# Kernel optimization log

Measured on AMD Instinct MI355X. Metric: run time of the kernel, lower is better.

## Reference

```python
import jax, jax.numpy as jnp
import numpy as np

H, DH = 12, 64
EPS = 1e-6
ROPE_BASE = 100.0

def rms_norm(x, scale=None, eps=EPS):
    xf = x.astype(jnp.float32)
    n = xf * jax.lax.rsqrt(jnp.mean(xf * xf, axis=-1, keepdims=True) + eps)
    if scale is not None:
        n = n * scale.astype(jnp.float32)
    return n.astype(x.dtype)

def rotate_half(x):
    h = x.shape[-1] // 2
    return jnp.concatenate([-x[..., h:], x[..., :h]], axis=-1)

def rope_cos_sin(pos_ids, head_dim, base=ROPE_BASE):
    # pos_ids: [B, N, 2] int -> cos/sin [B, N, head_dim]
    dim = head_dim // 2
    inv = 1.0 / base ** (jnp.arange(0, dim, 2, dtype=jnp.float32) / dim)  # [dim//2]
    cos_l, sin_l = [], []
    for i in range(2):  # x and y coordinate
        pos = pos_ids[:, :, i].astype(jnp.float32)           # [B, N]
        freqs = pos[:, :, None] * inv[None, None, :]          # [B, N, dim//2]
        emb = jnp.concatenate([freqs, freqs], axis=-1)        # [B, N, dim]
        cos_l.append(jnp.cos(emb))
        sin_l.append(jnp.sin(emb))
    return jnp.concatenate(cos_l, axis=-1), jnp.concatenate(sin_l, axis=-1)

def apply_2d_rope(x, cos, sin):
    # x: [B, N, H, Dh]; cos/sin: [B, N, Dh]; split channels evenly between x/y.
    c = x.shape[-1] // 2
    outs = []
    for k in range(2):
        xs = x[..., k * c:(k + 1) * c]
        cc = cos[:, :, None, k * c:(k + 1) * c]
        ss = sin[:, :, None, k * c:(k + 1) * c]
        outs.append(xs * cc + rotate_half(xs) * ss)
    return jnp.concatenate(outs, axis=-1)

def setup_inputs() -> dict:
    key = jax.random.key(0)
    ks = jax.random.split(key, 7)
    B, N, D = 8, 1024, 768
    hidden_states = jax.random.normal(ks[0], (B, N, D), dtype=jnp.float32)
    pixel_position_ids = jax.random.randint(ks[1], (B, N, 2), 0, 32, dtype=jnp.int32)
    s = 0.02
    Wq = jax.random.normal(ks[2], (H * DH, D), dtype=jnp.float32) * s
    Wk = jax.random.normal(ks[3], (H * DH, D), dtype=jnp.float32) * s
    Wv = jax.random.normal(ks[4], (H * DH, D), dtype=jnp.float32) * s
    Wo = jax.random.normal(ks[5], (D, H * DH), dtype=jnp.float32) * s
    q_scale = jnp.ones((DH,), dtype=jnp.float32)
    k_scale = jnp.ones((DH,), dtype=jnp.float32)
    return {"hidden_states": hidden_states, "pixel_position_ids": pixel_position_ids,
            "Wq": Wq, "Wk": Wk, "Wv": Wv, "Wo": Wo,
            "q_scale": q_scale, "k_scale": k_scale}

def reference(hidden_states, pixel_position_ids, Wq, Wk, Wv, Wo, q_scale, k_scale):
    B, N, D = hidden_states.shape
    # QKV projections (clip bounds are +/-inf -> no-op). Weights are [out, in].
    q = (hidden_states @ Wq.T).reshape(B, N, H, DH)
    k = (hidden_states @ Wk.T).reshape(B, N, H, DH)
    v = (hidden_states @ Wv.T).reshape(B, N, H, DH)
    # Per-head RMSNorm (v has no learned scale)
    q = rms_norm(q, q_scale)
    k = rms_norm(k, k_scale)
    v = rms_norm(v, None)
    # 2D RoPE
    cos, sin = rope_cos_sin(pixel_position_ids, DH)
    q = apply_2d_rope(q, cos, sin)
    k = apply_2d_rope(k, cos, sin)
    # Full attention, scaling = 1.0, softmax in fp32
    scores = jnp.einsum('bqhd,bkhd->bhqk', q, k)
    attn = jax.nn.softmax(scores.astype(jnp.float32), axis=-1).astype(q.dtype)
    out = jnp.einsum('bhqk,bkhd->bqhd', attn, v).reshape(B, N, H * DH)
    return out @ Wo.T
```

## Files before the change

### kernel.cpp

```cpp
#include <hip/hip_runtime.h>

typedef _Float16 f16;
typedef __attribute__((ext_vector_type(8))) _Float16 f16x8;
typedef __attribute__((ext_vector_type(4))) _Float16 f16x4;
typedef __attribute__((ext_vector_type(2))) __fp16 h16x2;
typedef __attribute__((ext_vector_type(4))) float f32x4;

#define NH 12
#define DHD 64
#define NB 8
#define NSEQ 1024
#define DMODEL 768
#define BHN (NB*NH)
#define ROWS_PER (BHN*NSEQ)

#define MFMA(a,b,c) __builtin_amdgcn_mfma_f32_16x16x32_f16(a,b,c,0,0,0)

__device__ __forceinline__ void gload16(const void* g, void* l) {
  __builtin_amdgcn_global_load_lds(
      (__attribute__((address_space(1))) void*)(g),
      (__attribute__((address_space(3))) void*)(l), 16, 0, 0);
}

__global__ __launch_bounds__(256) void cast_all_kernel(const float* __restrict__ hs,
                                                       const float* __restrict__ Wq,
                                                       const float* __restrict__ Wk,
                                                       const float* __restrict__ Wv,
                                                       const float* __restrict__ Wo,
                                                       f16* __restrict__ Xf,
                                                       f16* __restrict__ Wf,
                                                       f16* __restrict__ Wof,
                                                       float2* __restrict__ rtab,
                                                       int nhs, int nw) {
  int i = (blockIdx.x * blockDim.x + threadIdx.x) * 4;
  const float* src;
  f16* dst;
  if (i < nhs) {
    src = hs + i; dst = Xf + i;
  } else {
    int j = i - nhs;
    int which = j / nw;
    int off = j - which*nw;
    src = ((which == 0) ? Wq : (which == 1) ? Wk : (which == 2) ? Wv : Wo) + off;
    dst = ((which < 3) ? (Wf + (size_t)which*nw) : Wof) + off;
  }
  float4 v = *(const float4*)src;
  f16x4 o = {(f16)v.x, (f16)v.y, (f16)v.z, (f16)v.w};
  *(f16x4*)dst = o;
  if (blockIdx.x == 0) {
    for (int e = threadIdx.x; e < 512; e += 256) {
      int pos = e >> 4, k = e & 15;
      float ang = (float)pos * __expf((float)k * (-4.605170185988091f / 16.0f));
      float sn, cs;
      __sincosf(ang, &sn, &cs);
      rtab[e] = make_float2(cs, sn);
    }
  }
}

template<int MODE>
__global__ __launch_bounds__(512) void gemm_bt(const f16* __restrict__ A,
                                               const f16* __restrict__ B,
                                               float* __restrict__ Cout,
                                               f16* __restrict__ QKout,
                                               f16* __restrict__ Vout,
                                               const int* __restrict__ pos_ids,
                                               const float* __restrict__ q_scale,
                                               const float* __restrict__ k_scale,
                                               const float2* __restrict__ rtab,
                                               int M, int N, int K) {
  constexpr int BN = (MODE == 1) ? 128 : 64;
  constexpr int NJ = BN / 32;
  constexpr int ABUF = 8192;
  constexpr int BBUF = BN*64;
  __shared__ __align__(16) f16 SH[2*ABUF + 2*BBUF];
  const int tid = threadIdx.x;
  const int w = tid >> 6, l = tid & 63;
  const int wr = w >> 1, wc = w & 1;
  const int g = l >> 4, i16 = l & 15;

  int bx, by;
  {
    int id = blockIdx.x;
    const int nbx = (MODE == 1) ? 18 : 12;
    const int chunk = (MODE == 1) ? 144 : 96;
    int idp = (id & 7) * chunk + (id >> 3);
    by = idp / nbx; bx = idp - by * nbx;
  }

  const f32x4 fzero = {0.f, 0.f, 0.f, 0.f};
  f32x4 acc[2][NJ];
#pragma unroll
  for (int i = 0; i < 2; i++)
#pragma unroll
    for (int j = 0; j < NJ; j++) acc[i][j] = fzero;

  const int srow = tid >> 3;
  const int schunk = (tid & 7) ^ (srow & 7);
  const size_t arow = (size_t)(by*128 + srow)*K + schunk*8;
  const size_t brow = (size_t)(bx*BN + srow)*K + schunk*8;

  const int nt = K / 64;
#define STAGE(buf, k0)                                                          \
  {                                                                             \
    char* AlB = (char*)(SH + (buf)*ABUF) + w*1024;                              \
    char* BlB = (char*)(SH + 2*ABUF + (buf)*BBUF) + w*1024;                     \
    _Pragma("unroll")                                                           \
    for (int n = 0; n < 2; ++n)                                                 \
      gload16(A + arow + (size_t)(n*64)*K + (k0), AlB + n*8192);                \
    _Pragma("unroll")                                                           \
    for (int n = 0; n < BN/64; ++n)                                             \
      gload16(B + brow + (size_t)(n*64)*K + (k0), BlB + n*8192);                \
  }

  STAGE(0, 0);
  __syncthreads();
  for (int t = 0; t < nt; ++t) {
    const int buf = t & 1;
    if (t + 1 < nt) STAGE(buf ^ 1, (t + 1)*64);
    const f16* Ac = SH + buf*ABUF;
    const f16* Bc = SH + 2*ABUF + buf*BBUF;
#pragma unroll
    for (int kk = 0; kk < 2; ++kk) {
      f16x8 af[2], bfr[NJ];
#pragma unroll
      for (int i = 0; i < 2; i++)
        af[i] = *(const f16x8*)(Ac + (wr*32 + i*16 + i16)*64 + ((kk*4 + g) ^ (i16 & 7))*8);
#pragma unroll
      for (int j = 0; j < NJ; j++)
        bfr[j] = *(const f16x8*)(Bc + (wc*(BN/2) + j*16 + i16)*64 + ((kk*4 + g) ^ (i16 & 7))*8);
#pragma unroll
      for (int i = 0; i < 2; i++)
#pragma unroll
        for (int j = 0; j < NJ; j++)
          acc[i][j] = MFMA(af[i], bfr[j], acc[i][j]);
    }
    __syncthreads();
  }
#undef STAGE

  const int m0 = by*128 + wr*32;
  const int n0 = bx*BN + wc*(BN/2);
  if constexpr (MODE == 0) {
#pragma unroll
    for (int i = 0; i < 2; i++)
#pragma unroll
      for (int j = 0; j < NJ; j++)
#pragma unroll
        for (int r = 0; r < 4; r++) {
          int m = m0 + i*16 + g*4 + r;
          int n = n0 + j*16 + i16;
          Cout[(size_t)m*N + n] = acc[i][j][r];
        }
  } else {
  if (bx >= 12) {
    const int h0 = (bx - 12)*2;
    const int bb = by >> 3;
    const int ns0 = (by & 7) * 128;
    f16* Lt = SH;
#pragma unroll
    for (int i = 0; i < 2; i++) {
      f32x4 ssv = fzero;
#pragma unroll
      for (int j = 0; j < 4; j++)
#pragma unroll
        for (int r = 0; r < 4; r++) ssv[r] += acc[i][j][r]*acc[i][j][r];
#pragma unroll
      for (int d = 1; d < 16; d <<= 1)
#pragma unroll
        for (int r = 0; r < 4; r++) ssv[r] += __shfl_xor(ssv[r], d);
#pragma unroll
      for (int r = 0; r < 4; r++) {
        float rinv = rsqrtf(ssv[r] * (1.0f/64.0f) + 1e-6f);
        int nsl = wr*32 + i*16 + g*4 + r;
#pragma unroll
        for (int j = 0; j < 4; j++)
          Lt[(wc*64 + j*16 + i16)*136 + nsl] = (f16)(acc[i][j][r]*rinv);
      }
    }
    __syncthreads();
    const int dh = tid >> 2, q4 = tid & 3;
    f16* dst = Vout + ((size_t)((bb*NH + h0 + (dh >> 6))*64 + (dh & 63)))*1024
               + ns0 + q4*32;
    const f16* ls = Lt + dh*136 + q4*32;
#pragma unroll
    for (int e = 0; e < 4; ++e)
      *(uint4*)(dst + e*8) = *(const uint4*)(ls + e*8);
  } else {
    const int qkv = n0 / DMODEL;
    const int h = (n0 - qkv*DMODEL) >> 6;
    const float* scp = (qkv == 0) ? q_scale : k_scale;
    float scl[4];
#pragma unroll
    for (int j = 0; j < 4; j++) {
      scl[j] = scp[j*16 + i16];
      if (qkv == 0) scl[j] *= 1.4426950408889634f;
    }
    const float2* rt = rtab + i16;
#pragma unroll
    for (int i = 0; i < 2; i++) {
      f32x4 ssv = fzero;
#pragma unroll
      for (int j = 0; j < 4; j++)
#pragma unroll
        for (int r = 0; r < 4; r++) ssv[r] += acc[i][j][r]*acc[i][j][r];
#pragma unroll
      for (int d = 1; d < 16; d <<= 1)
#pragma unroll
        for (int r = 0; r < 4; r++) ssv[r] += __shfl_xor(ssv[r], d);
#pragma unroll
      for (int r = 0; r < 4; r++) {
        int m = m0 + i*16 + g*4 + r;
        int bb = m >> 10, ns = m & 1023;
        float rinv = rsqrtf(ssv[r] * (1.0f/64.0f) + 1e-6f);
        int2 pp = *(const int2*)(pos_ids + ((size_t)bb*NSEQ + ns)*2);
        float2 t0 = rt[pp.x*16];
        float2 t1 = rt[pp.y*16];
        float x0 = acc[i][0][r]*rinv*scl[0];
        float x1 = acc[i][1][r]*rinv*scl[1];
        float x2 = acc[i][2][r]*rinv*scl[2];
        float x3 = acc[i][3][r]*rinv*scl[3];
        size_t row = ((size_t)qkv*BHN + bb*NH + h)*NSEQ + ns;
        f16* ob = QKout + row*64;
        ob[i16]      = (f16)(x0*t0.x - x1*t0.y);
        ob[16 + i16] = (f16)(x1*t0.x + x0*t0.y);
        ob[32 + i16] = (f16)(x2*t1.x - x3*t1.y);
        ob[48 + i16] = (f16)(x3*t1.x + x2*t1.y);
      }
    }
  }
  }
}

__device__ __forceinline__ int sigma_perm(int p) {
  return (p & 0x20) | ((p & 0xC) << 1) | ((p & 0x10) >> 2) | (p & 3);
}

#define FM3(a,b,c) fmaxf(fmaxf(a,b),c)

__global__ __launch_bounds__(512) void attn_kernel(const f16* __restrict__ QKu,
                                                   const f16* __restrict__ Vtu,
                                                   f16* __restrict__ O) {
  const int id = blockIdx.x;
  const int xcd = id & 7, idx = id >> 3;
  const int bh = xcd*12 + (idx >> 3);
  const int q0 = (idx & 7) * 128;
  const int tid = threadIdx.x, w = tid >> 6, l = tid & 63;
  const int g = l >> 4, i16 = l & 15;
  const int g4 = g*4;
  const int sw = i16 & 7;
  const int b = bh / NH, h = bh - b*NH;

  __shared__ __align__(16) f16 Ks[2*64*64];
  __shared__ __align__(16) f16 Vs[2*64*64];

  const f16* qrow = QKu + ((size_t)bh*NSEQ + q0 + w*16 + i16)*64;
  f16x8 q0f = *(const f16x8*)(qrow + g*8);
  f16x8 q1f = *(const f16x8*)(qrow + 32 + g*8);

  const char* Kb  = (const char*)(QKu + (size_t)(BHN + bh)*NSEQ*64);
  const char* Vtb = (const char*)(Vtu + (size_t)bh*64*1024);
  const int prow0 = w*8 + (l >> 3);
  const int cl = (l & 7) ^ (l >> 3);
  const char* Ksrc = Kb + sigma_perm(prow0)*128 + cl*16;
  const char* Vsrc = Vtb + prow0*2048 + cl*16;

  const f32x4 fzero = {0.f, 0.f, 0.f, 0.f};
  const f16x8 vones = {(f16)1.f,(f16)1.f,(f16)1.f,(f16)1.f,
                       (f16)1.f,(f16)1.f,(f16)1.f,(f16)1.f};
  float mR = -1e30f;
  f32x4 o[4];
  f32x4 acc_l = fzero;
#pragma unroll
  for (int t = 0; t < 4; t++) o[t] = fzero;

  int cur = 0;
  {
    gload16(Ksrc, (char*)Ks + w*1024);
    gload16(Vsrc, (char*)Vs + w*1024);
  }
  __syncthreads();

  for (int t = 0; t < 16; ++t) {
    if (t < 15) {
      gload16(Ksrc + (t+1)*8192, (char*)Ks + (cur^1)*8192 + w*1024);
      gload16(Vsrc + (t+1)*128,  (char*)Vs + (cur^1)*8192 + w*1024);
    }
    const f16* Kc = Ks + cur*4096;
    const f16* Vc = Vs + cur*4096;

    f32x4 s[4] = {fzero, fzero, fzero, fzero};
    __builtin_amdgcn_s_setprio(1);
#pragma unroll
    for (int j = 0; j < 4; ++j) {
      const f16* kr = Kc + (j*16 + i16)*64;
      f16x8 k0 = *(const f16x8*)(kr + (g ^ sw)*8);
      f16x8 k1 = *(const f16x8*)(kr + ((g^4) ^ sw)*8);
      s[j] = MFMA(k0, q0f, s[j]);
      s[j] = MFMA(k1, q1f, s[j]);
    }
    __builtin_amdgcn_s_setprio(0);

    float t0m = FM3(s[0][0], s[0][1], s[0][2]);
    float t1m = FM3(s[0][3], s[1][0], s[1][1]);
    float t2m = FM3(s[1][2], s[1][3], s[2][0]);
    float t3m = FM3(s[2][1], s[2][2], s[2][3]);
    float t4m = FM3(s[3][0], s[3][1], s[3][2]);
    float tm = fmaxf(FM3(FM3(t0m, t1m, t2m), t3m, t4m), s[3][3]);
    tm = fmaxf(tm, __shfl_xor(tm, 16));
    tm = fmaxf(tm, __shfl_xor(tm, 32));
    if (__any(tm > mR + 11.5416f)) {
      float nm = fmaxf(mR, tm);
      float fac = __builtin_amdgcn_exp2f(mR - nm);
      mR = nm;
#pragma unroll
      for (int r = 0; r < 4; ++r) {
        float fr = __shfl(fac, g4 + r);
        o[0][r] *= fr; o[1][r] *= fr; o[2][r] *= fr; o[3][r] *= fr;
        acc_l[r] *= fr;
      }
    }
#pragma unroll
    for (int j = 0; j < 4; ++j)
#pragma unroll
      for (int r = 0; r < 4; ++r) s[j][r] = __builtin_amdgcn_exp2f(s[j][r] - mR);

    union { h16x2 h[4]; f16x8 v; } u0, u1;
    u0.h[0] = __builtin_amdgcn_cvt_pkrtz(s[0][0], s[0][1]);
    u0.h[1] = __builtin_amdgcn_cvt_pkrtz(s[0][2], s[0][3]);
    u0.h[2] = __builtin_amdgcn_cvt_pkrtz(s[1][0], s[1][1]);
    u0.h[3] = __builtin_amdgcn_cvt_pkrtz(s[1][2], s[1][3]);
    u1.h[0] = __builtin_amdgcn_cvt_pkrtz(s[2][0], s[2][1]);
    u1.h[1] = __builtin_amdgcn_cvt_pkrtz(s[2][2], s[2][3]);
    u1.h[2] = __builtin_amdgcn_cvt_pkrtz(s[3][0], s[3][1]);
    u1.h[3] = __builtin_amdgcn_cvt_pkrtz(s[3][2], s[3][3]);
    f16x8 pa0 = u0.v, pa1 = u1.v;

    __builtin_amdgcn_s_setprio(1);
#pragma unroll
    for (int t2 = 0; t2 < 4; ++t2) {
      const f16* vr = Vc + (t2*16 + i16)*64;
      f16x8 bv0 = *(const f16x8*)(vr + (g ^ sw)*8);
      f16x8 bv1 = *(const f16x8*)(vr + ((g^4) ^ sw)*8);
      o[t2] = MFMA(pa0, bv0, o[t2]);
      o[t2] = MFMA(pa1, bv1, o[t2]);
    }
    acc_l = MFMA(pa0, vones, acc_l);
    acc_l = MFMA(pa1, vones, acc_l);
    __builtin_amdgcn_s_setprio(0);

    __syncthreads();
    cur ^= 1;
  }

#pragma unroll
  for (int r = 0; r < 4; ++r) {
    float invl = 1.0f / acc_l[r];
    int q = q0 + w*16 + g4 + r;
    size_t base = ((size_t)(b*NSEQ + q))*DMODEL + h*DHD;
#pragma unroll
    for (int t2 = 0; t2 < 4; ++t2)
      O[base + t2*16 + i16] = (f16)(o[t2][r] * invl);
  }
}

extern "C" void kernel_launch(void* const* d_in, const int* in_sizes, int n_in,
                              void* d_out, int out_size, void* d_ws, size_t ws_size,
                              hipStream_t stream) {
  const float* hs = (const float*)d_in[0];
  const int*   pos = (const int*)d_in[1];
  const float* Wq = (const float*)d_in[2];
  const float* Wk = (const float*)d_in[3];
  const float* Wv = (const float*)d_in[4];
  const float* Wo = (const float*)d_in[5];
  const float* qs = (const float*)d_in[6];
  const float* ks = (const float*)d_in[7];

  const int nhs = 8192*768;
  const int nw  = 768*768;

  char* p = (char*)d_ws;
  f16* Xf   = (f16*)p; p += (size_t)nhs*2;
  f16* Wf   = (f16*)p; p += (size_t)3*nw*2;
  f16* Wof  = (f16*)p; p += (size_t)nw*2;
  f16* QKpk = (f16*)p; p += (size_t)2*ROWS_PER*64*2;
  f16* Vt   = (f16*)p; p += (size_t)ROWS_PER*64*2;
  f16* Ob   = (f16*)p; p += (size_t)nhs*2;
  float2* Rtab = (float2*)p; p += 512*sizeof(float2);

  cast_all_kernel<<<(nhs + 4*nw)/1024, 256, 0, stream>>>(hs, Wq, Wk, Wv, Wo,
                                                         Xf, Wf, Wof, Rtab, nhs, nw);

  gemm_bt<1><<<1152, 512, 0, stream>>>(Xf, Wf, nullptr, QKpk, Vt,
                                       pos, qs, ks, Rtab, 8192, 2304, 768);
  attn_kernel<<<768, 512, 0, stream>>>(QKpk, Vt, Ob);
  gemm_bt<0><<<768, 512, 0, stream>>>(Ob, Wof, (float*)d_out, nullptr, nullptr,
                                      nullptr, nullptr, nullptr, nullptr, 8192, 768, 768);
}
```

Baseline: 111.3 us.

## Triple-buffer QKV GEMM LDS pipeline with explicit vmcnt waits

For the QKV projection GEMM (MODE 1), the shared-memory staging goes from double to triple buffering. Two tiles are prefetched ahead, and waits are done with explicit s_waitcnt vmcnt(4) plus raw barriers in place of __syncthreads. This lets global-to-LDS loads for tile t+2 overlap compute on tile t and avoids draining all outstanding loads every iteration. It raises LDS usage per block, which may lower occupancy, and it relies on hand-counted vmcnt values being correct.

```diff
diff --git a/kernel.cpp b/kernel.cpp
--- a/kernel.cpp
+++ b/kernel.cpp
@@ -73,7 +73,8 @@
   constexpr int NJ = BN / 32;
   constexpr int ABUF = 8192;
   constexpr int BBUF = BN*64;
-  __shared__ __align__(16) f16 SH[2*ABUF + 2*BBUF];
+  constexpr int NBUF = (MODE == 1) ? 3 : 2;
+  __shared__ __align__(16) f16 SH[NBUF*(ABUF + BBUF)];
   const int tid = threadIdx.x;
   const int w = tid >> 6, l = tid & 63;
   const int wr = w >> 1, wc = w & 1;
@@ -104,7 +105,7 @@
 #define STAGE(buf, k0)                                                          \
   {                                                                             \
     char* AlB = (char*)(SH + (buf)*ABUF) + w*1024;                              \
-    char* BlB = (char*)(SH + 2*ABUF + (buf)*BBUF) + w*1024;                     \
+    char* BlB = (char*)(SH + NBUF*ABUF + (buf)*BBUF) + w*1024;                  \
     _Pragma("unroll")                                                           \
     for (int n = 0; n < 2; ++n)                                                 \
       gload16(A + arow + (size_t)(n*64)*K + (k0), AlB + n*8192);                \
@@ -112,32 +113,62 @@
     for (int n = 0; n < BN/64; ++n)                                             \
       gload16(B + brow + (size_t)(n*64)*K + (k0), BlB + n*8192);                \
   }
-
-  STAGE(0, 0);
-  __syncthreads();
-  for (int t = 0; t < nt; ++t) {
-    const int buf = t & 1;
-    if (t + 1 < nt) STAGE(buf ^ 1, (t + 1)*64);
-    const f16* Ac = SH + buf*ABUF;
-    const f16* Bc = SH + 2*ABUF + buf*BBUF;
-#pragma unroll
-    for (int kk = 0; kk < 2; ++kk) {
-      f16x8 af[2], bfr[NJ];
-#pragma unroll
-      for (int i = 0; i < 2; i++)
-        af[i] = *(const f16x8*)(Ac + (wr*32 + i*16 + i16)*64 + ((kk*4 + g) ^ (i16 & 7))*8);
-#pragma unroll
-      for (int j = 0; j < NJ; j++)
-        bfr[j] = *(const f16x8*)(Bc + (wc*(BN/2) + j*16 + i16)*64 + ((kk*4 + g) ^ (i16 & 7))*8);
-#pragma unroll
-      for (int i = 0; i < 2; i++)
-#pragma unroll
-        for (int j = 0; j < NJ; j++)
-          acc[i][j] = MFMA(af[i], bfr[j], acc[i][j]);
-    }
+#define COMPUTE(buf)                                                            \
+  {                                                                             \
+    const f16* Ac = SH + (buf)*ABUF;                                            \
+    const f16* Bc = SH + NBUF*ABUF + (buf)*BBUF;                                \
+    _Pragma("unroll")                                                           \
+    for (int kk = 0; kk < 2; ++kk) {                                            \
+      f16x8 af[2], bfr[NJ];                                                     \
+      _Pragma("unroll")                                                         \
+      for (int i = 0; i < 2; i++)                                               \
+        af[i] = *(const f16x8*)(Ac + (wr*32 + i*16 + i16)*64 +                  \
+                                ((kk*4 + g) ^ (i16 & 7))*8);                    \
+      _Pragma("unroll")                                                         \
+      for (int j = 0; j < NJ; j++)                                              \
+        bfr[j] = *(const f16x8*)(Bc + (wc*(BN/2) + j*16 + i16)*64 +             \
+                                 ((kk*4 + g) ^ (i16 & 7))*8);                   \
+      _Pragma("unroll")                                                         \
+      for (int i = 0; i < 2; i++)                                               \
+        _Pragma("unroll")                                                       \
+        for (int j = 0; j < NJ; j++)                                            \
+          acc[i][j] = MFMA(af[i], bfr[j], acc[i][j]);                           \
+    }                                                                           \
+  }
+
+  if constexpr (MODE == 1) {
+    STAGE(0, 0);
+    STAGE(1, 64);
+    asm volatile("s_waitcnt vmcnt(4)" ::: "memory");
+    __builtin_amdgcn_s_barrier();
+    __builtin_amdgcn_sched_barrier(0);
+    int b0 = 0, b1 = 1, b2 = 2;
+    for (int t = 0; t < nt - 2; ++t) {
+      STAGE(b2, (t + 2)*64);
+      COMPUTE(b0);
+      asm volatile("s_waitcnt vmcnt(4) lgkmcnt(0)" ::: "memory");
+      __builtin_amdgcn_s_barrier();
+      __builtin_amdgcn_sched_barrier(0);
+      int tmp = b0; b0 = b1; b1 = b2; b2 = tmp;
+    }
+    COMPUTE(b0);
+    asm volatile("s_waitcnt vmcnt(0) lgkmcnt(0)" ::: "memory");
+    __builtin_amdgcn_s_barrier();
+    __builtin_amdgcn_sched_barrier(0);
+    COMPUTE(b1);
     __syncthreads();
+  } else {
+    STAGE(0, 0);
+    __syncthreads();
+    for (int t = 0; t < nt; ++t) {
+      const int buf = t & 1;
+      if (t + 1 < nt) STAGE(buf ^ 1, (t + 1)*64);
+      COMPUTE(buf);
+      __syncthreads();
+    }
   }
 #undef STAGE
+#undef COMPUTE
 
   const int m0 = by*128 + wr*32;
   const int n0 = bx*BN + wc*(BN/2);
```

After: 120.1 us. 7.9% more time.
